# Optimization experiments

Measured on AMD Instinct MI355X. Metric: run time of the kernel, lower is better.

Reference implementation:

```python
import jax, jax.numpy as jnp
import numpy as np

NS, NH, NL, NP, E = 2, 8, 4, 4, 256
HD = E // NH  # 32


def grid_sample_zeros(img, grid):
    """torch.F.grid_sample(mode='bilinear', padding_mode='zeros', align_corners=False).
    img: [B, C, Hs, Ws]; grid: [B, Hg, Wg, 2] with (x, y) in [-1, 1]. Returns [B, C, Hg, Wg]."""
    B, C, Hs, Ws = img.shape
    gx = (grid[..., 0] + 1.0) * (Ws * 0.5) - 0.5  # pixel-space x
    gy = (grid[..., 1] + 1.0) * (Hs * 0.5) - 0.5  # pixel-space y
    x0 = jnp.floor(gx)
    y0 = jnp.floor(gy)
    x1, y1 = x0 + 1.0, y0 + 1.0
    wx1 = gx - x0
    wx0 = 1.0 - wx1
    wy1 = gy - y0
    wy0 = 1.0 - wy1
    imgf = img.reshape(B, C, Hs * Ws)

    def gather(ix, iy):
        valid = (ix >= 0) & (ix < Ws) & (iy >= 0) & (iy < Hs)
        ixc = jnp.clip(ix, 0, Ws - 1).astype(jnp.int32)
        iyc = jnp.clip(iy, 0, Hs - 1).astype(jnp.int32)
        flat = (iyc * Ws + ixc).reshape(B, 1, -1)
        vals = jnp.take_along_axis(imgf, flat, axis=2).reshape(B, C, *ix.shape[1:])
        return vals * valid[:, None].astype(img.dtype)

    return (gather(x0, y0) * (wx0 * wy0)[:, None]
            + gather(x1, y0) * (wx1 * wy0)[:, None]
            + gather(x0, y1) * (wx0 * wy1)[:, None]
            + gather(x1, y1) * (wx1 * wy1)[:, None])


def setup_inputs() -> dict:
    key = jax.random.key(0)
    ks = jax.random.split(key, 10)
    bs, Q = 2048, NL * NP  # num_query forced to num_levels*num_points = 16
    f = jnp.float32
    s = 1.0 / np.sqrt(E)
    return {
        "query": jax.random.normal(ks[0], (bs, Q, E), f),
        "key_hist": jax.random.normal(ks[1], (bs, Q, E), f),
        "value_hist": jax.random.normal(ks[2], (bs, Q, E), f),
        "reference_points": jax.random.uniform(ks[3], (bs, Q, NL, 2), f),
        "spatial_shapes": jnp.full((NL, 2), 2, dtype=jnp.int32),  # each level 2x2, sum HW = 16
        "Wq": jax.random.normal(ks[4], (E, E), f) * s, "bq": jnp.zeros((E,), f),
        "Wk": jax.random.normal(ks[5], (E, E), f) * s, "bk": jnp.zeros((E,), f),
        "Wv": jax.random.normal(ks[6], (E, E), f) * s, "bv": jnp.zeros((E,), f),
        "Woff": jax.random.normal(ks[7], (E, NH * NL * NP * 2), f) * (0.01 * s), "boff": jnp.zeros((NH * NL * NP * 2,), f),
        "Wout": jax.random.normal(ks[8], (E, E), f) * s, "bout": jnp.zeros((E,), f),
    }


def reference(query, key_hist, value_hist, reference_points, spatial_shapes,
              Wq, bq, Wk, bk, Wv, bv, Woff, boff, Wout, bout):
    bs, Q, _ = query.shape
    B = bs * NS
    residual = query

    # torch cat(dim=1)+view interleaves the two sequences per batch: index 2b -> query, 2b+1 -> hist
    queries = jnp.repeat(query, NS, axis=0)                              # [B, Q, E]
    keys = jnp.stack([query, key_hist], axis=1).reshape(B, Q, E)
    values = jnp.stack([query, value_hist], axis=1).reshape(B, Q, E)
    rp = jnp.repeat(reference_points, NS, axis=0)                        # [B, Q, NL, 2] (both copies identical)

    qh = (queries @ Wq + bq).reshape(B, Q, NH, HD)
    kh = (keys @ Wk + bk).reshape(B, Q, NH, HD)
    vh = (values @ Wv + bv).reshape(B, Q, NH, HD)

    attn = jax.nn.softmax(jnp.einsum('bqhd,bkhd->bqhk', qh, kh), axis=-1)
    attn = attn.reshape(B, Q, NH, NL, NP)

    offsets = (queries @ Woff + boff).reshape(B, Q, NH, NL, NP, 2)
    norm = jnp.stack([spatial_shapes[:, 1], spatial_shapes[:, 0]], axis=-1).astype(query.dtype)  # (W, H)
    loc = rp[:, :, None, :, None, :] + offsets / norm[None, None, None, :, None, :]
    grid = 2.0 * loc - 1.0                                               # [B, Q, NH, NL, NP, 2]

    ss = np.asarray(spatial_shapes)                                      # static level shapes
    attw = attn.transpose(0, 2, 1, 3, 4).reshape(B * NH, Q, NL, NP)      # [BH, Q, NL, NP]
    acc = jnp.zeros((B * NH, HD, Q), dtype=query.dtype)
    start = 0
    for l in range(NL):
        H_, W_ = int(ss[l, 0]), int(ss[l, 1])
        hw = H_ * W_
        v_l = vh[:, start:start + hw].transpose(0, 2, 3, 1).reshape(B * NH, HD, H_, W_)
        g_l = grid[:, :, :, l].transpose(0, 2, 1, 3, 4).reshape(B * NH, Q, NP, 2)
        s_l = grid_sample_zeros(v_l, g_l)                                # [BH, HD, Q, NP]
        acc = acc + jnp.sum(s_l * attw[:, None, :, l, :], axis=-1)       # weighted reduce over points
        start += hw

    out = acc.reshape(B, E, Q).transpose(0, 2, 1)                        # [B, Q, E]
    out = out.reshape(bs, NS, Q, E).mean(axis=1)                         # mean over the two sequences
    return out @ Wout + bout + residual                                  # dropout is identity in eval
```

## Files before the change

kernel.cpp:

```cpp
#include <hip/hip_runtime.h>

typedef float  f32x4  __attribute__((ext_vector_type(4)));
typedef __bf16 bf16x8 __attribute__((ext_vector_type(8)));
typedef __bf16 bf16x4 __attribute__((ext_vector_type(4)));

__device__ __forceinline__ bf16x8 cvt8(float4 a, float4 b) {
    bf16x8 r;
    r[0] = (__bf16)a.x; r[1] = (__bf16)a.y; r[2] = (__bf16)a.z; r[3] = (__bf16)a.w;
    r[4] = (__bf16)b.x; r[5] = (__bf16)b.y; r[6] = (__bf16)b.z; r[7] = (__bf16)b.w;
    return r;
}

#define OF_OFF 524288
#define PV_OFF (1u << 20)

#define SCRB 7680
#define QH   0
#define KH0  1280
#define KH1  2560
#define VT   3840
#define OFS  6400

__global__ void wprep(const float* __restrict__ Wq, const float* __restrict__ Wk,
                      const float* __restrict__ Wv, const float* __restrict__ Woff,
                      const float* __restrict__ Wout, __bf16* __restrict__ ws) {
    int id = blockIdx.x * 256 + threadIdx.x;
    if (id < 262144) {
        int tile = id >> 9, e = id & 511;
        int lane = e >> 3, j = e & 7;
        int kt = tile & 7, nh = (tile >> 3) & 1, mat = (tile >> 4) & 3, h = tile >> 6;
        int k = kt * 32 + (lane >> 4) * 8 + j;
        int col = h * 32 + nh * 16 + (lane & 15);
        const float* W = (mat == 0) ? Wq : (mat == 1) ? Wk : (mat == 2) ? Wv : Woff;
        ws[id] = (__bf16)W[k * 256 + col];
    } else {
        int i = id - 262144;
        int tile = i >> 9, e = i & 511;
        int lane = e >> 3, j = e & 7;
        int kt = tile & 7, nt = tile >> 3;
        int k = kt * 32 + (lane >> 4) * 8 + j;
        int col = nt * 16 + (lane & 15);
        ws[262144 + i] = (__bf16)Wout[k * 256 + col];
    }
}

__launch_bounds__(512, 4)
__global__ void tsa_one(const float* __restrict__ query, const float* __restrict__ keyh,
                        const float* __restrict__ valh, const float* __restrict__ refpts,
                        unsigned char* __restrict__ wsw,
                        const float* __restrict__ bq, const float* __restrict__ bk,
                        const float* __restrict__ bv, const float* __restrict__ boff,
                        const float* __restrict__ bout, float* __restrict__ out, int b0)
{
    __shared__ __attribute__((aligned(16))) unsigned char uni[16384];
    __shared__ __attribute__((aligned(16))) unsigned char scr_all[4 * SCRB];
    __shared__ __attribute__((aligned(16))) unsigned char vfr[32768];
    const int t = threadIdx.x;
    const int lane = t & 63, w = t >> 6, l15 = lane & 15, lhi = lane >> 4;
    const int p = w >> 1;
    const int role = w & 1;
    const long b = (long)b0 + (long)blockIdx.x * 4 + p;
    unsigned char* scrp = scr_all + p * SCRB;
    unsigned char* vfrp = vfr + p * 8192;
    __bf16* pvg = (__bf16*)(wsw + PV_OFF) + ((long)blockIdx.x * 4 + p) * 4096;

    bf16x8 afr[8];
    {
        const float* s0 = (role ? keyh : query) + b * 4096 + l15 * 256;
        #pragma unroll
        for (int kt = 0; kt < 8; ++kt) {
            int o = kt * 32 + lhi * 8;
            afr[kt] = cvt8(*(const float4*)(s0 + o), *(const float4*)(s0 + o + 4));
        }
        if (role) {
            const float* s1 = valh + b * 4096 + l15 * 256;
            #pragma unroll
            for (int kt = 0; kt < 8; ++kt) {
                int o = kt * 32 + lhi * 8;
                *(bf16x8*)(vfrp + kt * 1024 + lane * 16) =
                    cvt8(*(const float4*)(s1 + o), *(const float4*)(s1 + o + 4));
            }
        }
    }
    const f32x4 z = (f32x4){0.f, 0.f, 0.f, 0.f};
    float2 rp = *(const float2*)(refpts + b * 128 + l15 * 8 + lhi * 2);
    __syncthreads();

    for (int h = 0; h < 8; ++h) {
        #pragma unroll 2
        for (int nh = 0; nh < 2; ++nh) {
            f32x4 acc[4];
            #pragma unroll
            for (int i = 0; i < 4; ++i) acc[i] = z;
            #pragma unroll 2
            for (int half = 0; half < 2; ++half) {
                __syncthreads();
                #pragma unroll
                for (int it = 0; it < 2; ++it) {
                    int u = t + it * 512;
                    int f = u >> 6;
                    int kt = (half << 2) + (f & 3);
                    const void* src = (const void*)(wsw +
                        ((((h * 4 + (f >> 2)) * 2 + nh) * 8 + kt) << 10) + (u & 63) * 16);
                    __builtin_amdgcn_global_load_lds(
                        (const __attribute__((address_space(1))) unsigned int*)src,
                        (__attribute__((address_space(3))) unsigned int*)(uni + u * 16),
                        16, 0, 0);
                }
                __syncthreads();
                __builtin_amdgcn_s_setprio(1);
                #pragma unroll
                for (int ktl = 0; ktl < 4; ++ktl) {
                    int kt = (half << 2) + ktl;
                    const unsigned char* bb = uni + ktl * 1024 + lane * 16;
                    bf16x8 b_k = *(const bf16x8*)(bb + 4096);
                    bf16x8 b_v = *(const bf16x8*)(bb + 8192);
                    if (!role) {
                        bf16x8 b_q = *(const bf16x8*)(bb);
                        bf16x8 b_o = *(const bf16x8*)(bb + 12288);
                        acc[0] = __builtin_amdgcn_mfma_f32_16x16x32_bf16(afr[kt], b_q, acc[0], 0, 0, 0);
                        acc[1] = __builtin_amdgcn_mfma_f32_16x16x32_bf16(afr[kt], b_k, acc[1], 0, 0, 0);
                        acc[2] = __builtin_amdgcn_mfma_f32_16x16x32_bf16(afr[kt], b_v, acc[2], 0, 0, 0);
                        acc[3] = __builtin_amdgcn_mfma_f32_16x16x32_bf16(afr[kt], b_o, acc[3], 0, 0, 0);
                    } else {
                        bf16x8 av = *(const bf16x8*)(vfrp + kt * 1024 + lane * 16);
                        acc[0] = __builtin_amdgcn_mfma_f32_16x16x32_bf16(afr[kt], b_k, acc[0], 0, 0, 0);
                        acc[1] = __builtin_amdgcn_mfma_f32_16x16x32_bf16(av,      b_v, acc[1], 0, 0, 0);
                    }
                }
                __builtin_amdgcn_s_setprio(0);
            }
            {
                int dcol = nh * 16 + l15;
                int gcol = h * 32 + dcol;
                if (!role) {
                    float bqv = bq[gcol], bkv = bk[gcol], bvv = bv[gcol], bov = boff[gcol];
                    #pragma unroll
                    for (int r = 0; r < 4; ++r) {
                        int row = lhi * 4 + r;
                        *(__bf16*)(scrp + QH  + row * 80 + dcol * 2) = (__bf16)(acc[0][r] + bqv);
                        *(__bf16*)(scrp + KH0 + row * 80 + dcol * 2) = (__bf16)(acc[1][r] + bkv);
                        *(__bf16*)(scrp + VT  + dcol * 80 + row * 2) = (__bf16)(acc[2][r] + bvv);
                        *(__bf16*)(scrp + OFS + row * 80 + dcol * 2) = (__bf16)(acc[3][r] + bov);
                    }
                } else {
                    float bkv = bk[gcol], bvv = bv[gcol];
                    #pragma unroll
                    for (int r = 0; r < 4; ++r) {
                        int row = lhi * 4 + r;
                        *(__bf16*)(scrp + KH1 + row * 80 + dcol * 2)      = (__bf16)(acc[0][r] + bkv);
                        *(__bf16*)(scrp + VT  + dcol * 80 + 32 + row * 2) = (__bf16)(acc[1][r] + bvv);
                    }
                }
            }
        }
        __syncthreads();

        bf16x8 qf = *(const bf16x8*)(scrp + QH + l15 * 80 + lhi * 16);
        bf16x8 kf = *(const bf16x8*)(scrp + KH0 + role * 1280 + l15 * 80 + lhi * 16);
        f32x4 S = __builtin_amdgcn_mfma_f32_16x16x32_bf16(kf, qf, z, 0, 0, 0);
        float pr4[4];
        {
            float m = fmaxf(fmaxf(S[0], S[1]), fmaxf(S[2], S[3]));
            m = fmaxf(m, __shfl_xor(m, 16)); m = fmaxf(m, __shfl_xor(m, 32));
            float s = 0.f;
            #pragma unroll
            for (int r = 0; r < 4; ++r) { pr4[r] = __expf(S[r] - m); s += pr4[r]; }
            s += __shfl_xor(s, 16); s += __shfl_xor(s, 32);
            float inv = 1.f / s;
            #pragma unroll
            for (int r = 0; r < 4; ++r) pr4[r] *= inv;
        }

        {
            bf16x8 off8 = *(const bf16x8*)(scrp + OFS + l15 * 80 + lhi * 16);
            float w4[4] = {0.f, 0.f, 0.f, 0.f};
            #pragma unroll
            for (int pp = 0; pp < 4; ++pp) {
                float gx = 2.f * rp.x + (float)off8[2 * pp]     - 0.5f;
                float gy = 2.f * rp.y + (float)off8[2 * pp + 1] - 0.5f;
                float tx0 = fmaxf(0.f, 1.f - fabsf(gx));
                float tx1 = fmaxf(0.f, 1.f - fabsf(gx - 1.f));
                float ty0 = fmaxf(0.f, 1.f - fabsf(gy));
                float ty1 = fmaxf(0.f, 1.f - fabsf(gy - 1.f));
                w4[0] += tx0 * ty0 * pr4[pp]; w4[1] += tx1 * ty0 * pr4[pp];
                w4[2] += tx0 * ty1 * pr4[pp]; w4[3] += tx1 * ty1 * pr4[pp];
            }
            *(bf16x4*)(scrp + KH0 + role * 1280 + l15 * 80 + lhi * 8) =
                (bf16x4){(__bf16)w4[0], (__bf16)w4[1], (__bf16)w4[2], (__bf16)w4[3]};
        }
        __syncthreads();

        {
            bf16x8 aW = *(const bf16x8*)(scrp + KH0 + (lhi >> 1) * 1280 + l15 * 80 + (lhi & 1) * 16);
            bf16x8 vf = *(const bf16x8*)(scrp + VT + (role * 16 + l15) * 80 + lhi * 16);
            f32x4 c4 = __builtin_amdgcn_mfma_f32_16x16x32_bf16(aW, vf, z, 0, 0, 0);
            #pragma unroll
            for (int r = 0; r < 4; ++r) {
                int qq = lhi * 4 + r;
                *(__bf16*)(scrp + QH + qq * 80 + (role * 16 + l15) * 2) = (__bf16)(0.5f * c4[r]);
            }
        }
        __syncthreads();
        if (!role) {
            bf16x8 pvfrag = *(const bf16x8*)(scrp + QH + l15 * 80 + lhi * 16);
            *(bf16x8*)(pvg + h * 512 + lane * 8) = pvfrag;
        }
    }

    __syncthreads();

    {
        bf16x8 pv[8];
        #pragma unroll
        for (int kt = 0; kt < 8; ++kt)
            pv[kt] = *(const bf16x8*)(pvg + kt * 512 + lane * 8);
        for (int qd = 0; qd < 4; ++qd) {
            f32x4 o2[2];
            o2[0] = z; o2[1] = z;
            #pragma unroll
            for (int kt = 0; kt < 8; ++kt) {
                #pragma unroll
                for (int j = 0; j < 2; ++j) {
                    int ntl = role * 2 + j;
                    bf16x8 bfr = *(const bf16x8*)(wsw + OF_OFF + qd * 32768 +
                                                  (ntl * 8 + kt) * 1024 + lane * 16);
                    o2[j] = __builtin_amdgcn_mfma_f32_16x16x32_bf16(pv[kt], bfr, o2[j], 0, 0, 0);
                }
            }
            #pragma unroll
            for (int j = 0; j < 2; ++j) {
                int ntl = role * 2 + j;
                int col = (qd * 4 + ntl) * 16 + l15;
                float bo = bout[col];
                #pragma unroll
                for (int r = 0; r < 4; ++r) {
                    int qq = lhi * 4 + r;
                    long idx = b * 4096 + qq * 256 + col;
                    out[idx] = o2[j][r] + bo + query[idx];
                }
            }
        }
    }
}

extern "C" void kernel_launch(void* const* d_in, const int* in_sizes, int n_in,
                              void* d_out, int out_size, void* d_ws, size_t ws_size,
                              hipStream_t stream) {
    const float* query      = (const float*)d_in[0];
    const float* key_hist   = (const float*)d_in[1];
    const float* value_hist = (const float*)d_in[2];
    const float* refpts     = (const float*)d_in[3];
    const float* Wq   = (const float*)d_in[5];
    const float* bq   = (const float*)d_in[6];
    const float* Wk   = (const float*)d_in[7];
    const float* bk   = (const float*)d_in[8];
    const float* Wv   = (const float*)d_in[9];
    const float* bv   = (const float*)d_in[10];
    const float* Woff = (const float*)d_in[11];
    const float* boff = (const float*)d_in[12];
    const float* Wout = (const float*)d_in[13];
    const float* bout = (const float*)d_in[14];
    float* outp = (float*)d_out;

    const int bs = in_sizes[0] / 4096;
    wprep<<<1280, 256, 0, stream>>>(Wq, Wk, Wv, Woff, Wout, (__bf16*)d_ws);

    long avail = (long)ws_size - (long)PV_OFF;
    int CB = bs;
    if (avail < (long)bs * 8192) {
        CB = (int)(avail / 8192) & ~3;
        if (CB < 4) CB = 4;
    }
    for (int b0 = 0; b0 < bs; b0 += CB) {
        int nb = (bs - b0 < CB ? bs - b0 : CB) / 4;
        tsa_one<<<nb, 512, 0, stream>>>(query, key_hist, value_hist, refpts,
                                        (unsigned char*)d_ws,
                                        bq, bk, bv, boff, bout, outp, b0);
    }
}
```

Before: 84.62 us.

## Software-pipeline weight staging into LDS to overlap with MFMA and attention

Restructures the per-head projection loop so each global-to-LDS weight tile load is issued right after the previous tile's compute. The next head's first tile is prefetched before the attention/sampling phase. This hides global-load latency behind scatter and attention work and cuts the number of block-wide barriers per head. It relies on the later phases not touching the staging buffer while the prefetch is in flight, which makes the synchronisation more fragile.

```diff
diff --git a/kernel.cpp b/kernel.cpp
--- a/kernel.cpp
+++ b/kernel.cpp
@@ -65,6 +65,70 @@
     __bf16* pvg = (__bf16*)(wsw + PV_OFF) + ((long)blockIdx.x * 4 + p) * 4096;
 
     bf16x8 afr[8];
+
+    auto stage16 = [&](int h, int nh, int half) {
+        #pragma unroll
+        for (int it = 0; it < 2; ++it) {
+            int u = t + it * 512;
+            int f = u >> 6;
+            int kt = (half << 2) + (f & 3);
+            const void* src = (const void*)(wsw +
+                ((((h * 4 + (f >> 2)) * 2 + nh) * 8 + kt) << 10) + (u & 63) * 16);
+            __builtin_amdgcn_global_load_lds(
+                (const __attribute__((address_space(1))) unsigned int*)src,
+                (__attribute__((address_space(3))) unsigned int*)(uni + u * 16),
+                16, 0, 0);
+        }
+    };
+
+    auto burst = [&](int half, f32x4* acc) {
+        __builtin_amdgcn_s_setprio(1);
+        #pragma unroll
+        for (int ktl = 0; ktl < 4; ++ktl) {
+            int kt = (half << 2) + ktl;
+            const unsigned char* bb = uni + ktl * 1024 + lane * 16;
+            bf16x8 b_k = *(const bf16x8*)(bb + 4096);
+            bf16x8 b_v = *(const bf16x8*)(bb + 8192);
+            if (!role) {
+                bf16x8 b_q = *(const bf16x8*)(bb);
+                bf16x8 b_o = *(const bf16x8*)(bb + 12288);
+                acc[0] = __builtin_amdgcn_mfma_f32_16x16x32_bf16(afr[kt], b_q, acc[0], 0, 0, 0);
+                acc[1] = __builtin_amdgcn_mfma_f32_16x16x32_bf16(afr[kt], b_k, acc[1], 0, 0, 0);
+                acc[2] = __builtin_amdgcn_mfma_f32_16x16x32_bf16(afr[kt], b_v, acc[2], 0, 0, 0);
+                acc[3] = __builtin_amdgcn_mfma_f32_16x16x32_bf16(afr[kt], b_o, acc[3], 0, 0, 0);
+            } else {
+                bf16x8 av = *(const bf16x8*)(vfrp + kt * 1024 + lane * 16);
+                acc[0] = __builtin_amdgcn_mfma_f32_16x16x32_bf16(afr[kt], b_k, acc[0], 0, 0, 0);
+                acc[1] = __builtin_amdgcn_mfma_f32_16x16x32_bf16(av,      b_v, acc[1], 0, 0, 0);
+            }
+        }
+        __builtin_amdgcn_s_setprio(0);
+    };
+
+    auto scatter = [&](int h, int nh, const f32x4* acc) {
+        int dcol = nh * 16 + l15;
+        int gcol = h * 32 + dcol;
+        if (!role) {
+            float bqv = bq[gcol], bkv = bk[gcol], bvv = bv[gcol], bov = boff[gcol];
+            #pragma unroll
+            for (int r = 0; r < 4; ++r) {
+                int row = lhi * 4 + r;
+                *(__bf16*)(scrp + QH  + row * 80 + dcol * 2) = (__bf16)(acc[0][r] + bqv);
+                *(__bf16*)(scrp + KH0 + row * 80 + dcol * 2) = (__bf16)(acc[1][r] + bkv);
+                *(__bf16*)(scrp + VT  + dcol * 80 + row * 2) = (__bf16)(acc[2][r] + bvv);
+                *(__bf16*)(scrp + OFS + row * 80 + dcol * 2) = (__bf16)(acc[3][r] + bov);
+            }
+        } else {
+            float bkv = bk[gcol], bvv = bv[gcol];
+            #pragma unroll
+            for (int r = 0; r < 4; ++r) {
+                int row = lhi * 4 + r;
+                *(__bf16*)(scrp + KH1 + row * 80 + dcol * 2)      = (__bf16)(acc[0][r] + bkv);
+                *(__bf16*)(scrp + VT  + dcol * 80 + 32 + row * 2) = (__bf16)(acc[1][r] + bvv);
+            }
+        }
+    };
+
     {
         const float* s0 = (role ? keyh : query) + b * 4096 + l15 * 256;
         #pragma unroll
@@ -84,77 +148,33 @@
     }
     const f32x4 z = (f32x4){0.f, 0.f, 0.f, 0.f};
     float2 rp = *(const float2*)(refpts + b * 128 + l15 * 8 + lhi * 2);
+
+    stage16(0, 0, 0);
     __syncthreads();
 
     for (int h = 0; h < 8; ++h) {
-        #pragma unroll 2
-        for (int nh = 0; nh < 2; ++nh) {
-            f32x4 acc[4];
-            #pragma unroll
-            for (int i = 0; i < 4; ++i) acc[i] = z;
-            #pragma unroll 2
-            for (int half = 0; half < 2; ++half) {
-                __syncthreads();
-                #pragma unroll
-                for (int it = 0; it < 2; ++it) {
-                    int u = t + it * 512;
-                    int f = u >> 6;
-                    int kt = (half << 2) + (f & 3);
-                    const void* src = (const void*)(wsw +
-                        ((((h * 4 + (f >> 2)) * 2 + nh) * 8 + kt) << 10) + (u & 63) * 16);
-                    __builtin_amdgcn_global_load_lds(
-                        (const __attribute__((address_space(1))) unsigned int*)src,
-                        (__attribute__((address_space(3))) unsigned int*)(uni + u * 16),
-                        16, 0, 0);
-                }
-                __syncthreads();
-                __builtin_amdgcn_s_setprio(1);
-                #pragma unroll
-                for (int ktl = 0; ktl < 4; ++ktl) {
-                    int kt = (half << 2) + ktl;
-                    const unsigned char* bb = uni + ktl * 1024 + lane * 16;
-                    bf16x8 b_k = *(const bf16x8*)(bb + 4096);
-                    bf16x8 b_v = *(const bf16x8*)(bb + 8192);
-                    if (!role) {
-                        bf16x8 b_q = *(const bf16x8*)(bb);
-                        bf16x8 b_o = *(const bf16x8*)(bb + 12288);
-                        acc[0] = __builtin_amdgcn_mfma_f32_16x16x32_bf16(afr[kt], b_q, acc[0], 0, 0, 0);
-                        acc[1] = __builtin_amdgcn_mfma_f32_16x16x32_bf16(afr[kt], b_k, acc[1], 0, 0, 0);
-                        acc[2] = __builtin_amdgcn_mfma_f32_16x16x32_bf16(afr[kt], b_v, acc[2], 0, 0, 0);
-                        acc[3] = __builtin_amdgcn_mfma_f32_16x16x32_bf16(afr[kt], b_o, acc[3], 0, 0, 0);
-                    } else {
-                        bf16x8 av = *(const bf16x8*)(vfrp + kt * 1024 + lane * 16);
-                        acc[0] = __builtin_amdgcn_mfma_f32_16x16x32_bf16(afr[kt], b_k, acc[0], 0, 0, 0);
-                        acc[1] = __builtin_amdgcn_mfma_f32_16x16x32_bf16(av,      b_v, acc[1], 0, 0, 0);
-                    }
-                }
-                __builtin_amdgcn_s_setprio(0);
-            }
-            {
-                int dcol = nh * 16 + l15;
-                int gcol = h * 32 + dcol;
-                if (!role) {
-                    float bqv = bq[gcol], bkv = bk[gcol], bvv = bv[gcol], bov = boff[gcol];
-                    #pragma unroll
-                    for (int r = 0; r < 4; ++r) {
-                        int row = lhi * 4 + r;
-                        *(__bf16*)(scrp + QH  + row * 80 + dcol * 2) = (__bf16)(acc[0][r] + bqv);
-                        *(__bf16*)(scrp + KH0 + row * 80 + dcol * 2) = (__bf16)(acc[1][r] + bkv);
-                        *(__bf16*)(scrp + VT  + dcol * 80 + row * 2) = (__bf16)(acc[2][r] + bvv);
-                        *(__bf16*)(scrp + OFS + row * 80 + dcol * 2) = (__bf16)(acc[3][r] + bov);
-                    }
-                } else {
-                    float bkv = bk[gcol], bvv = bv[gcol];
-                    #pragma unroll
-                    for (int r = 0; r < 4; ++r) {
-                        int row = lhi * 4 + r;
-                        *(__bf16*)(scrp + KH1 + row * 80 + dcol * 2)      = (__bf16)(acc[0][r] + bkv);
-                        *(__bf16*)(scrp + VT  + dcol * 80 + 32 + row * 2) = (__bf16)(acc[1][r] + bvv);
-                    }
-                }
-            }
-        }
-        __syncthreads();
+        f32x4 acc[4];
+        #pragma unroll
+        for (int i = 0; i < 4; ++i) acc[i] = z;
+        burst(0, acc);
+        __syncthreads();
+        stage16(h, 0, 1);
+        __syncthreads();
+        burst(1, acc);
+        __syncthreads();
+        stage16(h, 1, 0);
+        scatter(h, 0, acc);
+        __syncthreads();
+        #pragma unroll
+        for (int i = 0; i < 4; ++i) acc[i] = z;
+        burst(0, acc);
+        __syncthreads();
+        stage16(h, 1, 1);
+        __syncthreads();
+        burst(1, acc);
+        scatter(h, 1, acc);
+        __syncthreads();
+        if (h < 7) stage16(h + 1, 0, 0);
 
         bf16x8 qf = *(const bf16x8*)(scrp + QH + l15 * 80 + lhi * 16);
         bf16x8 kf = *(const bf16x8*)(scrp + KH0 + role * 1280 + l15 * 80 + lhi * 16);
```

Measured after the change: 79.94 us. 1.06x faster.
